# Kernel optimization log

Hardware: AMD Instinct MI355X
Metric: run time of the kernel (lower is better)

## Reference

```python
import jax, jax.numpy as jnp
import numpy as np

WS = 8        # window size (square)
HEADS = 8
DIM = 512
EPS = 1e-5


def _ln(x, g, b):
    m = x.mean(-1, keepdims=True)
    v = x.var(-1, keepdims=True)
    return (x - m) / jnp.sqrt(v + EPS) * g + b


def _bn(x, g, b, m, v):
    # eval-mode BatchNorm2d on NCHW
    sh = (1, -1, 1, 1)
    return (x - m.reshape(sh)) / jnp.sqrt(v.reshape(sh) + EPS) * g.reshape(sh) + b.reshape(sh)


def _win_rev(w, H, W, C):
    # (B*nW, WS*WS, C) -> (B, C, H, W)
    x = w.reshape(-1, H // WS, W // WS, WS, WS, C)
    return x.transpose(0, 5, 1, 3, 2, 4).reshape(-1, C, H, W)


def _win_part(x):
    # (B, C, H, W) -> (B*nW, WS*WS, C)
    B, C, H, W = x.shape
    x = x.reshape(B, C, H // WS, WS, W // WS, WS)
    return x.transpose(0, 2, 4, 3, 5, 1).reshape(-1, WS * WS, C)


def setup_inputs() -> dict:
    key = jax.random.key(0)
    ks = iter(jax.random.split(key, 64))
    def nrm(sh, s=0.02):
        return jax.random.normal(next(ks), sh, jnp.float32) * s
    C, C2, C8 = DIM, DIM // 2, DIM // 8
    B, H, W = 2, 224, 224
    N = WS * WS
    B_ = B * (H // WS) * (W // WS)
    # relative position index (same construction as the torch module)
    coords = np.stack(np.meshgrid(np.arange(WS), np.arange(WS), indexing='ij'))
    cf = coords.reshape(2, -1)
    rel = (cf[:, :, None] - cf[:, None, :]).transpose(1, 2, 0).astype(np.int64)
    rel[:, :, 0] += WS - 1
    rel[:, :, 1] += WS - 1
    rel[:, :, 0] *= 2 * WS - 1
    rel_idx = jnp.asarray(rel.sum(-1), jnp.int32)   # (N, N)
    ones = lambda n: jnp.ones((n,), jnp.float32)
    zeros = lambda n: jnp.zeros((n,), jnp.float32)
    return dict(
        x=jax.random.normal(next(ks), (B_, N, C), jnp.float32),
        w_pa=nrm((C, C2)), b_pa=zeros(C2),
        g_lna=ones(C2) + nrm((C2,), 0.1), b_lna=nrm((C2,), 0.1),
        w_pc=nrm((C, C)), b_pc=zeros(C),
        g_lnc=ones(C) + nrm((C,), 0.1), b_lnc=nrm((C,), 0.1),
        dw_w=nrm((C, 1, 3, 3), 0.1), dw_b=zeros(C),
        g_bn1=ones(C), b_bn1=zeros(C), m_bn1=nrm((C,), 0.1), v_bn1=ones(C),
        ci_w1=nrm((C, C8)), ci_b1=zeros(C8),
        g_bn2=ones(C8), b_bn2=zeros(C8), m_bn2=nrm((C8,), 0.1), v_bn2=ones(C8),
        ci_w2=nrm((C8, C2)), ci_b2=zeros(C2),
        pj_w=nrm((C, C2)), pj_b=zeros(C2),
        g_bn3=ones(C2), b_bn3=zeros(C2), m_bn3=nrm((C2,), 0.1), v_bn3=ones(C2),
        w_qkv=nrm((C2, 3 * C2)), b_qkv=zeros(3 * C2),
        si_w1=nrm((C2, C8)), si_b1=zeros(C8),
        g_bn4=ones(C8), b_bn4=zeros(C8), m_bn4=nrm((C8,), 0.1), v_bn4=ones(C8),
        si_w2=nrm((C8, 1)), si_b2=zeros(1),
        g_lno=ones(C2) + nrm((C2,), 0.1), b_lno=nrm((C2,), 0.1),
        w_out=nrm((C, C)), b_out=zeros(C),
        rpb=nrm(((2 * WS - 1) ** 2, HEADS)),
        rel_idx=rel_idx, H=H, W=W,
    )


def _forward(x, w_pa, b_pa, g_lna, b_lna, w_pc, b_pc, g_lnc, b_lnc,
             dw_w, dw_b, g_bn1, b_bn1, m_bn1, v_bn1,
             ci_w1, ci_b1, g_bn2, b_bn2, m_bn2, v_bn2, ci_w2, ci_b2,
             pj_w, pj_b, g_bn3, b_bn3, m_bn3, v_bn3,
             w_qkv, b_qkv,
             si_w1, si_b1, g_bn4, b_bn4, m_bn4, v_bn4, si_w2, si_b2,
             g_lno, b_lno, w_out, b_out, rpb, rel_idx, H, W):
    B_, N, C = x.shape
    C2 = C // 2
    hd = C2 // HEADS
    scale = hd ** -0.5
    x_att = _ln(x @ w_pa + b_pa, g_lna, b_lna)            # (B_, N, C2)
    x_cnn = _ln(x @ w_pc + b_pc, g_lnc, b_lnc)            # (B_, N, C)
    x_cnn = _win_rev(x_cnn, H, W, C)                      # (B, C, H, W)
    # depthwise 3x3 conv + BN + GELU
    x_cnn = jax.lax.conv_general_dilated(
        x_cnn, dw_w, (1, 1), [(1, 1), (1, 1)],
        feature_group_count=C, dimension_numbers=('NCHW', 'OIHW', 'NCHW')
    ) + dw_b.reshape(1, -1, 1, 1)
    x_cnn = jax.nn.gelu(_bn(x_cnn, g_bn1, b_bn1, m_bn1, v_bn1), approximate=False)
    # channel interaction: global avg pool -> 1x1 conv -> BN -> GELU -> 1x1 conv
    ci = x_cnn.mean((2, 3))                               # (B, C)
    ci = ci @ ci_w1 + ci_b1                               # (B, C/8)
    ci = jax.nn.gelu((ci - m_bn2) / jnp.sqrt(v_bn2 + EPS) * g_bn2 + b_bn2, approximate=False)
    ci = ci @ ci_w2 + ci_b2                               # (B, C2)
    x_cnn = jnp.einsum('bchw,co->bohw', x_cnn, pj_w) + pj_b.reshape(1, -1, 1, 1)  # (B, C2, H, W)
    # windowed multi-head attention
    qkv = (x_att @ w_qkv + b_qkv).reshape(B_, N, 3, HEADS, hd).transpose(2, 0, 3, 1, 4)
    q, k, v = qkv[0], qkv[1], qkv[2]                      # (B_, heads, N, hd)
    B = ci.shape[0]
    gate = jax.nn.sigmoid(ci).reshape(B, 1, HEADS, 1, hd)
    v = (v.reshape(B, -1, HEADS, N, hd) * gate).reshape(B_, HEADS, N, hd)
    attn = jnp.einsum('bhnd,bhmd->bhnm', q * scale, k)    # (B_, heads, N, N)
    bias = rpb[rel_idx[:N, :N].reshape(-1)].reshape(N, N, HEADS).transpose(2, 0, 1)
    attn = jax.nn.softmax(attn + bias[None], axis=-1)
    x_att = jnp.einsum('bhnm,bhmd->bnhd', attn, v).reshape(B_, N, C2)
    # spatial interaction gating of the conv branch
    x_sp = _win_rev(x_att, H, W, C2)                      # (B, C2, H, W)
    si = jnp.einsum('bchw,co->bohw', x_sp, si_w1) + si_b1.reshape(1, -1, 1, 1)
    si = jax.nn.gelu(_bn(si, g_bn4, b_bn4, m_bn4, v_bn4), approximate=False)
    si = jnp.einsum('bchw,co->bohw', si, si_w2) + si_b2.reshape(1, -1, 1, 1)      # (B, 1, H, W)
    x_cnn = _bn(jax.nn.sigmoid(si) * x_cnn, g_bn3, b_bn3, m_bn3, v_bn3)
    x_cnn = _win_part(x_cnn)                              # (B_, N, C2)
    x_att = _ln(x_att, g_lno, b_lno)
    return jnp.concatenate([x_att, x_cnn], axis=-1) @ w_out + b_out


def reference(x, w_pa, b_pa, g_lna, b_lna, w_pc, b_pc, g_lnc, b_lnc,
              dw_w, dw_b, g_bn1, b_bn1, m_bn1, v_bn1,
              ci_w1, ci_b1, g_bn2, b_bn2, m_bn2, v_bn2, ci_w2, ci_b2,
              pj_w, pj_b, g_bn3, b_bn3, m_bn3, v_bn3,
              w_qkv, b_qkv,
              si_w1, si_b1, g_bn4, b_bn4, m_bn4, v_bn4, si_w2, si_b2,
              g_lno, b_lno, w_out, b_out, rpb, rel_idx, H, W):
    return _forward(x, w_pa, b_pa, g_lna, b_lna, w_pc, b_pc, g_lnc, b_lnc,
                    dw_w, dw_b, g_bn1, b_bn1, m_bn1, v_bn1,
                    ci_w1, ci_b1, g_bn2, b_bn2, m_bn2, v_bn2, ci_w2, ci_b2,
                    pj_w, pj_b, g_bn3, b_bn3, m_bn3, v_bn3,
                    w_qkv, b_qkv,
                    si_w1, si_b1, g_bn4, b_bn4, m_bn4, v_bn4, si_w2, si_b2,
                    g_lno, b_lno, w_out, b_out, rpb, rel_idx, H, W)
```

## Files before the change

### kernel.cpp

```cpp
#include <hip/hip_runtime.h>
#include <math.h>

#define EPS 1e-5f
#define MROWS 100352
#define NWIN  1568

typedef __attribute__((ext_vector_type(8))) short bf16x8;
typedef __attribute__((ext_vector_type(4))) float f32x4;

__device__ __forceinline__ unsigned short f2bf(float f) {
  unsigned u = __float_as_uint(f);
  u += 0x7fffu + ((u >> 16) & 1u);
  return (unsigned short)(u >> 16);
}
__device__ __forceinline__ float bf2f(unsigned short s) {
  return __uint_as_float(((unsigned)s) << 16);
}
__device__ __forceinline__ float gelu_exact(float x) {
  return 0.5f * x * (1.f + erff(x * 0.70710678118654752f));
}

#define GLOAD16(gp, lp)                                              \
  __builtin_amdgcn_global_load_lds(                                  \
      (const __attribute__((address_space(1))) void*)(gp),           \
      (__attribute__((address_space(3))) void*)(lp), 16, 0, 0)

template <bool OUTBF>
__global__ __launch_bounds__(256) void gemm_bf16(
    const unsigned short* __restrict__ A, const unsigned short* __restrict__ Bt,
    const float* __restrict__ bias, void* __restrict__ Cout,
    int M, int N, int K) {
  __shared__ unsigned short As[128 * 32];
  __shared__ unsigned short Bs[128 * 32];
  const int tid = threadIdx.x;
  const int lane = tid & 63, wave = tid >> 6;
  const int wr = wave >> 1, wc = wave & 1;
  const int row0 = blockIdx.y * 128, col0 = blockIdx.x * 128;
  const int lrow = tid >> 2, loff = (tid & 3) * 8;
  f32x4 acc[4][4];
#pragma unroll
  for (int m = 0; m < 4; ++m)
#pragma unroll
    for (int n = 0; n < 4; ++n) acc[m][n] = (f32x4){0.f, 0.f, 0.f, 0.f};
  for (int k0 = 0; k0 < K; k0 += 32) {
    __syncthreads();
#pragma unroll
    for (int p = 0; p < 2; ++p) {
      int r = p * 64 + lrow;
      GLOAD16(&A[(size_t)(row0 + r) * K + k0 + loff], &As[r * 32 + loff]);
      GLOAD16(&Bt[(size_t)(col0 + r) * K + k0 + loff], &Bs[r * 32 + loff]);
    }
    __syncthreads();
    const int g8 = (lane >> 4) * 8, rl = lane & 15;
    bf16x8 af[4], bfr[4];
#pragma unroll
    for (int m = 0; m < 4; ++m)
      af[m] = *(const bf16x8*)&As[(wr * 64 + m * 16 + rl) * 32 + g8];
#pragma unroll
    for (int n = 0; n < 4; ++n)
      bfr[n] = *(const bf16x8*)&Bs[(wc * 64 + n * 16 + rl) * 32 + g8];
#pragma unroll
    for (int m = 0; m < 4; ++m)
#pragma unroll
      for (int n = 0; n < 4; ++n)
        acc[m][n] = __builtin_amdgcn_mfma_f32_16x16x32_bf16(af[m], bfr[n],
                                                            acc[m][n], 0, 0, 0);
  }
  const int crow = (lane >> 4) * 4, ccol = lane & 15;
#pragma unroll
  for (int n = 0; n < 4; ++n) {
    const int gc = col0 + wc * 64 + n * 16 + ccol;
    const float bz = bias[gc];
#pragma unroll
    for (int m = 0; m < 4; ++m) {
      const int gr0 = row0 + wr * 64 + m * 16 + crow;
#pragma unroll
      for (int r = 0; r < 4; ++r) {
        float val = acc[m][n][r] + bz;
        if constexpr (OUTBF)
          ((unsigned short*)Cout)[(size_t)(gr0 + r) * N + gc] = f2bf(val);
        else
          ((float*)Cout)[(size_t)(gr0 + r) * N + gc] = val;
      }
    }
  }
}

__global__ __launch_bounds__(256) void gemm_f32a(
    const float* __restrict__ A, const unsigned short* __restrict__ Bt,
    const float* __restrict__ bias, unsigned short* __restrict__ Cout,
    int M, int N, int K) {
  __shared__ unsigned short As[128 * 32];
  __shared__ unsigned short Bs[128 * 32];
  const int tid = threadIdx.x;
  const int lane = tid & 63, wave = tid >> 6;
  const int wr = wave >> 1, wc = wave & 1;
  const int row0 = blockIdx.y * 128, col0 = blockIdx.x * 128;
  const int lrow = tid >> 2, loff = (tid & 3) * 8;
  const int ar = tid >> 1, ac = (tid & 1) * 16;
  f32x4 acc[4][4];
#pragma unroll
  for (int m = 0; m < 4; ++m)
#pragma unroll
    for (int n = 0; n < 4; ++n) acc[m][n] = (f32x4){0.f, 0.f, 0.f, 0.f};
  for (int k0 = 0; k0 < K; k0 += 32) {
    float4 f[4];
#pragma unroll
    for (int i = 0; i < 4; ++i)
      f[i] = *(const float4*)&A[(size_t)(row0 + ar) * K + k0 + ac + i * 4];
    __syncthreads();
#pragma unroll
    for (int p = 0; p < 2; ++p) {
      int r = p * 64 + lrow;
      GLOAD16(&Bt[(size_t)(col0 + r) * K + k0 + loff], &Bs[r * 32 + loff]);
    }
#pragma unroll
    for (int i = 0; i < 4; ++i) {
      ushort4 u = make_ushort4(f2bf(f[i].x), f2bf(f[i].y), f2bf(f[i].z), f2bf(f[i].w));
      *(ushort4*)&As[ar * 32 + ac + i * 4] = u;
    }
    __syncthreads();
    const int g8 = (lane >> 4) * 8, rl = lane & 15;
    bf16x8 af[4], bfr[4];
#pragma unroll
    for (int m = 0; m < 4; ++m)
      af[m] = *(const bf16x8*)&As[(wr * 64 + m * 16 + rl) * 32 + g8];
#pragma unroll
    for (int n = 0; n < 4; ++n)
      bfr[n] = *(const bf16x8*)&Bs[(wc * 64 + n * 16 + rl) * 32 + g8];
#pragma unroll
    for (int m = 0; m < 4; ++m)
#pragma unroll
      for (int n = 0; n < 4; ++n)
        acc[m][n] = __builtin_amdgcn_mfma_f32_16x16x32_bf16(af[m], bfr[n],
                                                            acc[m][n], 0, 0, 0);
  }
  const int crow = (lane >> 4) * 4, ccol = lane & 15;
#pragma unroll
  for (int n = 0; n < 4; ++n) {
    const int gc = col0 + wc * 64 + n * 16 + ccol;
    const float bz = bias[gc];
#pragma unroll
    for (int m = 0; m < 4; ++m) {
      const int gr0 = row0 + wr * 64 + m * 16 + crow;
#pragma unroll
      for (int r = 0; r < 4; ++r)
        Cout[(size_t)(gr0 + r) * N + gc] = f2bf(acc[m][n][r] + bz);
    }
  }
}

__global__ __launch_bounds__(256) void wt_convert(const float* __restrict__ in,
                                                  unsigned short* __restrict__ out,
                                                  int K, int N) {
  int i = blockIdx.x * 256 + threadIdx.x;
  if (i >= K * N) return;
  int n = i / K, k = i - n * K;
  out[i] = f2bf(in[(size_t)k * N + n]);
}

__global__ __launch_bounds__(256) void pack_bias(const float* __restrict__ b_pa,
                                                 const float* __restrict__ b_pc,
                                                 float* __restrict__ out) {
  int t = blockIdx.x * 256 + threadIdx.x;
  if (t < 256) out[t] = b_pa[t];
  else if (t < 768) out[t] = b_pc[t - 256];
}

template <int W>
__global__ __launch_bounds__(256) void ln_rows_bf(
    const unsigned short* __restrict__ in, int istride,
    unsigned short* __restrict__ out,
    const float* __restrict__ g, const float* __restrict__ b) {
  const int row = blockIdx.x * 4 + (threadIdx.x >> 6);
  const int t = threadIdx.x & 63;
  constexpr int NE = W / 64;
  float v[NE];
  const size_t ibase = (size_t)row * istride + t * NE;
  const size_t obase = (size_t)row * W + t * NE;
#pragma unroll
  for (int c4 = 0; c4 < NE / 4; ++c4) {
    ushort4 u = *(const ushort4*)&in[ibase + c4 * 4];
    v[c4 * 4 + 0] = bf2f(u.x); v[c4 * 4 + 1] = bf2f(u.y);
    v[c4 * 4 + 2] = bf2f(u.z); v[c4 * 4 + 3] = bf2f(u.w);
  }
  float s = 0.f, sq = 0.f;
#pragma unroll
  for (int j = 0; j < NE; ++j) { s += v[j]; sq += v[j] * v[j]; }
#pragma unroll
  for (int off = 32; off >= 1; off >>= 1) {
    s += __shfl_xor(s, off);
    sq += __shfl_xor(sq, off);
  }
  const float mean = s * (1.f / W);
  const float var = sq * (1.f / W) - mean * mean;
  const float rstd = rsqrtf(var + EPS);
#pragma unroll
  for (int c4 = 0; c4 < NE / 4; ++c4) {
    int c = t * NE + c4 * 4;
    ushort4 o = make_ushort4(
        f2bf((v[c4 * 4 + 0] - mean) * rstd * g[c + 0] + b[c + 0]),
        f2bf((v[c4 * 4 + 1] - mean) * rstd * g[c + 1] + b[c + 1]),
        f2bf((v[c4 * 4 + 2] - mean) * rstd * g[c + 2] + b[c + 2]),
        f2bf((v[c4 * 4 + 3] - mean) * rstd * g[c + 3] + b[c + 3]));
    *(ushort4*)&out[obase + c4 * 4] = o;
  }
}

__global__ __launch_bounds__(256) void dwconv_bn_gelu(
    const unsigned short* __restrict__ xin, const float* __restrict__ wgt9,
    const float* __restrict__ dwb, const float* __restrict__ g1,
    const float* __restrict__ b1, const float* __restrict__ m1,
    const float* __restrict__ v1, unsigned short* __restrict__ outp,
    float* __restrict__ ci_part) {
  __shared__ unsigned short tile[100 * 128];
  __shared__ float psum[8 * 128];
  const int b_ = blockIdx.x;
  const int b = b_ / 784, win = b_ % 784;
  const int wi = win / 28, wj = win % 28;
  const int h0 = wi * 8 - 1, w0 = wj * 8 - 1;
  const int tid = threadIdx.x;
  const int c4 = (tid & 31) * 4;
  const int pg = tid >> 5;
  for (int chunk = 0; chunk < 4; ++chunk) {
    const int c0 = chunk * 128;
    __syncthreads();
#pragma unroll
    for (int it = 0; it < 7; ++it) {
      int idx = it * 256 + tid;
      if (idx < 1600) {
        int p = idx >> 4;
        int ch8 = (idx & 15) * 8;
        int ph = h0 + p / 10, pw = w0 + p % 10;
        uint4 val = {0u, 0u, 0u, 0u};
        if (ph >= 0 && ph < 224 && pw >= 0 && pw < 224) {
          int bs = b * 784 + (ph >> 3) * 28 + (pw >> 3);
          int n = ((ph & 7) << 3) | (pw & 7);
          val = *(const uint4*)&xin[(size_t)(bs * 64 + n) * 512 + c0 + ch8];
        }
        *(uint4*)&tile[p * 128 + ch8] = val;
      }
    }
    __syncthreads();
    float wreg[9][4];
    float scale[4], shift[4], bias0[4];
#pragma unroll
    for (int j = 0; j < 4; ++j) {
      int cc = c0 + c4 + j;
#pragma unroll
      for (int k = 0; k < 9; ++k) wreg[k][j] = wgt9[cc * 9 + k];
      scale[j] = g1[cc] * rsqrtf(v1[cc] + EPS);
      shift[j] = b1[cc] - m1[cc] * scale[j];
      bias0[j] = dwb[cc];
    }
    float cs0 = 0.f, cs1 = 0.f, cs2 = 0.f, cs3 = 0.f;
    for (int q = 0; q < 8; ++q) {
      const int qq = pg * 8 + q;
      const int r = qq >> 3, cc_ = qq & 7;
      float a0 = bias0[0], a1 = bias0[1], a2 = bias0[2], a3 = bias0[3];
#pragma unroll
      for (int dr = 0; dr < 3; ++dr)
#pragma unroll
        for (int dc = 0; dc < 3; ++dc) {
          ushort4 u = *(const ushort4*)&tile[((r + dr) * 10 + cc_ + dc) * 128 + c4];
          const int k = dr * 3 + dc;
          a0 += bf2f(u.x) * wreg[k][0];
          a1 += bf2f(u.y) * wreg[k][1];
          a2 += bf2f(u.z) * wreg[k][2];
          a3 += bf2f(u.w) * wreg[k][3];
        }
      float g0 = gelu_exact(a0 * scale[0] + shift[0]);
      float g1v = gelu_exact(a1 * scale[1] + shift[1]);
      float g2v = gelu_exact(a2 * scale[2] + shift[2]);
      float g3v = gelu_exact(a3 * scale[3] + shift[3]);
      cs0 += g0; cs1 += g1v; cs2 += g2v; cs3 += g3v;
      *(ushort4*)&outp[(size_t)(b_ * 64 + qq) * 512 + c0 + c4] =
          make_ushort4(f2bf(g0), f2bf(g1v), f2bf(g2v), f2bf(g3v));
    }
    *(float4*)&psum[pg * 128 + c4] = make_float4(cs0, cs1, cs2, cs3);
    __syncthreads();
    if (tid < 128) {
      float s = 0.f;
#pragma unroll
      for (int g = 0; g < 8; ++g) s += psum[g * 128 + tid];
      ci_part[(size_t)b_ * 512 + c0 + tid] = s;
    }
  }
}

__global__ __launch_bounds__(512) void ci_reduce(const float* __restrict__ ci_part,
                                                 float* __restrict__ ci_mean) {
  const int b = blockIdx.x, c = threadIdx.x;
  float s = 0.f;
  for (int w = 0; w < 784; ++w) s += ci_part[(size_t)(b * 784 + w) * 512 + c];
  ci_mean[b * 512 + c] = s * (1.f / 50176.f);
}

__global__ __launch_bounds__(512) void ci_gate(
    const float* __restrict__ ci_mean, const float* __restrict__ w1,
    const float* __restrict__ bi1, const float* __restrict__ g2,
    const float* __restrict__ b2, const float* __restrict__ m2,
    const float* __restrict__ v2, const float* __restrict__ w2,
    const float* __restrict__ bi2, float* __restrict__ gate) {
  __shared__ float cm[1024];
  __shared__ float c1[128];
  const int t = threadIdx.x;
  cm[t] = ci_mean[t];
  cm[t + 512] = ci_mean[t + 512];
  __syncthreads();
  if (t < 128) {
    int b = t >> 6, j = t & 63;
    float acc = bi1[j];
    for (int c = 0; c < 512; ++c) acc += cm[b * 512 + c] * w1[c * 64 + j];
    float sc = g2[j] * rsqrtf(v2[j] + EPS);
    c1[t] = gelu_exact((acc - m2[j]) * sc + b2[j]);
  }
  __syncthreads();
  {
    int b = t >> 8, o = t & 255;
    float acc = bi2[o];
#pragma unroll
    for (int j = 0; j < 64; ++j) acc += c1[b * 64 + j] * w2[j * 256 + o];
    gate[b * 256 + o] = 1.f / (1.f + expf(-acc));
  }
}

__global__ __launch_bounds__(256) void bias_pre(const float* __restrict__ rpb,
                                                const int* __restrict__ rel,
                                                float* __restrict__ biasf) {
  int i = blockIdx.x * 256 + threadIdx.x;
  if (i >= 4096) return;
  int r = rel[i];
#pragma unroll
  for (int h = 0; h < 8; ++h) biasf[h * 4096 + i] = rpb[r * 8 + h];
}

__global__ __launch_bounds__(256) void attn_mfma(
    const unsigned short* __restrict__ qkv,
    const float* __restrict__ gate,
    const float* __restrict__ biasf,
    unsigned short* __restrict__ outp) {
  __shared__ unsigned short lds[4 * (64 * 68 + 32 * 68)];
  const int w = blockIdx.x;
  const int b = w / 784;
  const int tid = threadIdx.x, lane = tid & 63, wave = tid >> 6;
  unsigned short* p_lds = lds + wave * (64 * 68 + 32 * 68);
  unsigned short* vT = p_lds + 64 * 68;
  const int l15 = lane & 15, l4 = lane >> 4;
  const float scale = 0.17677669529663687f;
  for (int hh = 0; hh < 2; ++hh) {
    const int h = wave * 2 + hh;
    {
      const float* gh = &gate[b * 256 + h * 32];
      const size_t vbase = ((size_t)w * 64 + lane) * 768 + 512 + h * 32;
#pragma unroll
      for (int c = 0; c < 4; ++c) {
        uint4 vv = *(const uint4*)&qkv[vbase + c * 8];
        float4 gA = *(const float4*)&gh[c * 8];
        float4 gB = *(const float4*)&gh[c * 8 + 4];
        unsigned vw[4] = {vv.x, vv.y, vv.z, vv.w};
        float gg[8] = {gA.x, gA.y, gA.z, gA.w, gB.x, gB.y, gB.z, gB.w};
#pragma unroll
        for (int j = 0; j < 4; ++j) {
          int d = c * 8 + j * 2;
          vT[(d + 0) * 68 + lane] = f2bf(__uint_as_float(vw[j] << 16) * gg[j * 2]);
          vT[(d + 1) * 68 + lane] =
              f2bf(__uint_as_float(vw[j] & 0xffff0000u) * gg[j * 2 + 1]);
        }
      }
    }
    bf16x8 kf[4], qf[4];
    const size_t qkbase = (size_t)w * 64 * 768 + h * 32 + l4 * 8;
#pragma unroll
    for (int t = 0; t < 4; ++t) {
      kf[t] = *(const bf16x8*)&qkv[qkbase + (size_t)(t * 16 + l15) * 768 + 256];
      qf[t] = *(const bf16x8*)&qkv[qkbase + (size_t)(t * 16 + l15) * 768];
    }
    f32x4 s[4][4];
#pragma unroll
    for (int mt = 0; mt < 4; ++mt)
#pragma unroll
      for (int nt = 0; nt < 4; ++nt) s[mt][nt] = (f32x4){0.f, 0.f, 0.f, 0.f};
#pragma unroll
    for (int mt = 0; mt < 4; ++mt)
#pragma unroll
      for (int nt = 0; nt < 4; ++nt)
        s[mt][nt] = __builtin_amdgcn_mfma_f32_16x16x32_bf16(kf[mt], qf[nt],
                                                            s[mt][nt], 0, 0, 0);
    float inv_s[4];
#pragma unroll
    for (int nt = 0; nt < 4; ++nt) {
      float mx = -1e30f;
#pragma unroll
      for (int mt = 0; mt < 4; ++mt) {
        float4 b4 = *(const float4*)&biasf[(h * 64 + nt * 16 + l15) * 64 +
                                           mt * 16 + l4 * 4];
        s[mt][nt][0] = s[mt][nt][0] * scale + b4.x;
        s[mt][nt][1] = s[mt][nt][1] * scale + b4.y;
        s[mt][nt][2] = s[mt][nt][2] * scale + b4.z;
        s[mt][nt][3] = s[mt][nt][3] * scale + b4.w;
#pragma unroll
        for (int r = 0; r < 4; ++r) mx = fmaxf(mx, s[mt][nt][r]);
      }
      mx = fmaxf(mx, __shfl_xor(mx, 16));
      mx = fmaxf(mx, __shfl_xor(mx, 32));
      float sum = 0.f;
#pragma unroll
      for (int mt = 0; mt < 4; ++mt)
#pragma unroll
        for (int r = 0; r < 4; ++r) {
          float e = __expf(s[mt][nt][r] - mx);
          s[mt][nt][r] = e;
          sum += e;
        }
      sum += __shfl_xor(sum, 16);
      sum += __shfl_xor(sum, 32);
      inv_s[nt] = 1.f / sum;
    }
#pragma unroll
    for (int nt = 0; nt < 4; ++nt)
#pragma unroll
      for (int mt = 0; mt < 4; ++mt) {
        ushort4 pk = make_ushort4(f2bf(s[mt][nt][0] * inv_s[nt]),
                                  f2bf(s[mt][nt][1] * inv_s[nt]),
                                  f2bf(s[mt][nt][2] * inv_s[nt]),
                                  f2bf(s[mt][nt][3] * inv_s[nt]));
        *(ushort4*)&p_lds[(nt * 16 + l15) * 68 + mt * 16 + l4 * 4] = pk;
      }
    f32x4 o[4][2];
#pragma unroll
    for (int i = 0; i < 4; ++i)
#pragma unroll
      for (int dt = 0; dt < 2; ++dt) o[i][dt] = (f32x4){0.f, 0.f, 0.f, 0.f};
#pragma unroll
    for (int ks = 0; ks < 2; ++ks) {
      bf16x8 pa[4], vf[2];
#pragma unroll
      for (int i = 0; i < 4; ++i) {
        const unsigned short* pp = &p_lds[(i * 16 + l15) * 68 + ks * 32 + l4 * 8];
        union { bf16x8 v; ushort4 u[2]; } tmp;
        tmp.u[0] = *(const ushort4*)pp;
        tmp.u[1] = *(const ushort4*)(pp + 4);
        pa[i] = tmp.v;
      }
#pragma unroll
      for (int dt = 0; dt < 2; ++dt) {
        const unsigned short* vp = &vT[(dt * 16 + l15) * 68 + ks * 32 + l4 * 8];
        union { bf16x8 v; ushort4 u[2]; } tmp;
        tmp.u[0] = *(const ushort4*)vp;
        tmp.u[1] = *(const ushort4*)(vp + 4);
        vf[dt] = tmp.v;
      }
#pragma unroll
      for (int i = 0; i < 4; ++i)
#pragma unroll
        for (int dt = 0; dt < 2; ++dt)
          o[i][dt] = __builtin_amdgcn_mfma_f32_16x16x32_bf16(pa[i], vf[dt],
                                                             o[i][dt], 0, 0, 0);
    }
#pragma unroll
    for (int i = 0; i < 4; ++i)
#pragma unroll
      for (int dt = 0; dt < 2; ++dt)
#pragma unroll
        for (int r = 0; r < 4; ++r)
          outp[((size_t)w * 64 + i * 16 + l4 * 4 + r) * 256 + h * 32 +
               dt * 16 + l15] = f2bf(o[i][dt][r]);
  }
}

__global__ __launch_bounds__(256) void si_ln_concat(
    const unsigned short* __restrict__ xatt, const unsigned short* __restrict__ xpj,
    const float* __restrict__ w1, const float* __restrict__ bi1,
    const float* __restrict__ g4, const float* __restrict__ b4v,
    const float* __restrict__ m4, const float* __restrict__ v4,
    const float* __restrict__ w2, const float* __restrict__ bi2,
    const float* __restrict__ g3, const float* __restrict__ b3v,
    const float* __restrict__ m3, const float* __restrict__ v3,
    const float* __restrict__ glno, const float* __restrict__ blno,
    unsigned short* __restrict__ outc) {
  __shared__ float xr[16 * 256];
  __shared__ float s1s[16 * 64];
  __shared__ float sig[16];
  const int t = threadIdx.x;
  const int row0 = blockIdx.x * 16;
#pragma unroll
  for (int i = 0; i < 2; ++i) {
    int idx = i * 256 + t;
    int pr = idx >> 5, pc = (idx & 31) * 8;
    const unsigned short* src = &xatt[(size_t)(row0 + pr) * 256 + pc];
    ushort4 a = *(const ushort4*)src;
    ushort4 c = *(const ushort4*)(src + 4);
    float* dst = &xr[pr * 256 + pc];
    dst[0] = bf2f(a.x); dst[1] = bf2f(a.y); dst[2] = bf2f(a.z); dst[3] = bf2f(a.w);
    dst[4] = bf2f(c.x); dst[5] = bf2f(c.y); dst[6] = bf2f(c.z); dst[7] = bf2f(c.w);
  }
  __syncthreads();
  {
    const int j = t & 63, pg = t >> 6;
    float acc[4];
    const float bj = bi1[j];
#pragma unroll
    for (int i = 0; i < 4; ++i) acc[i] = bj;
    for (int cc = 0; cc < 256; ++cc) {
      float wv = w1[cc * 64 + j];
#pragma unroll
      for (int i = 0; i < 4; ++i) acc[i] += xr[(pg * 4 + i) * 256 + cc] * wv;
    }
    const float sc4 = g4[j] * rsqrtf(v4[j] + EPS);
    const float m4j = m4[j], b4j = b4v[j];
#pragma unroll
    for (int i = 0; i < 4; ++i)
      s1s[(pg * 4 + i) * 64 + j] = gelu_exact((acc[i] - m4j) * sc4 + b4j);
  }
  __syncthreads();
  if (t < 16) {
    float a2 = bi2[0];
#pragma unroll
    for (int jj = 0; jj < 64; ++jj) a2 += s1s[t * 64 + jj] * w2[jj];
    sig[t] = 1.f / (1.f + expf(-a2));
  }
  __syncthreads();
  {
    const int p = t >> 4, l = t & 15;
    float4 v4s[4];
    float s = 0.f, sq = 0.f;
#pragma unroll
    for (int cq = 0; cq < 4; ++cq) {
      float4 x4 = *(const float4*)&xr[p * 256 + cq * 64 + l * 4];
      v4s[cq] = x4;
      s += x4.x + x4.y + x4.z + x4.w;
      sq += x4.x * x4.x + x4.y * x4.y + x4.z * x4.z + x4.w * x4.w;
    }
#pragma unroll
    for (int off = 8; off >= 1; off >>= 1) {
      s += __shfl_xor(s, off);
      sq += __shfl_xor(sq, off);
    }
    const float mean = s * (1.f / 256.f);
    const float var = sq * (1.f / 256.f) - mean * mean;
    const float rstd = rsqrtf(var + EPS);
    const size_t orow = (size_t)(row0 + p) * 512;
#pragma unroll
    for (int cq = 0; cq < 4; ++cq) {
      int c = cq * 64 + l * 4;
      float4 x4 = v4s[cq];
      *(ushort4*)&outc[orow + c] = make_ushort4(
          f2bf((x4.x - mean) * rstd * glno[c + 0] + blno[c + 0]),
          f2bf((x4.y - mean) * rstd * glno[c + 1] + blno[c + 1]),
          f2bf((x4.z - mean) * rstd * glno[c + 2] + blno[c + 2]),
          f2bf((x4.w - mean) * rstd * glno[c + 3] + blno[c + 3]));
    }
    const float sg = sig[p];
#pragma unroll
    for (int cq = 0; cq < 4; ++cq) {
      int c = cq * 64 + l * 4;
      ushort4 pu = *(const ushort4*)&xpj[(size_t)(row0 + p) * 256 + c];
      float px = bf2f(pu.x), py = bf2f(pu.y), pz = bf2f(pu.z), pw = bf2f(pu.w);
      float sc0 = g3[c + 0] * rsqrtf(v3[c + 0] + EPS);
      float sc1 = g3[c + 1] * rsqrtf(v3[c + 1] + EPS);
      float sc2 = g3[c + 2] * rsqrtf(v3[c + 2] + EPS);
      float sc3 = g3[c + 3] * rsqrtf(v3[c + 3] + EPS);
      *(ushort4*)&outc[orow + 256 + c] = make_ushort4(
          f2bf(sg * px * sc0 + (b3v[c + 0] - m3[c + 0] * sc0)),
          f2bf(sg * py * sc1 + (b3v[c + 1] - m3[c + 1] * sc1)),
          f2bf(sg * pz * sc2 + (b3v[c + 2] - m3[c + 2] * sc2)),
          f2bf(sg * pw * sc3 + (b3v[c + 3] - m3[c + 3] * sc3)));
    }
  }
}

extern "C" void kernel_launch(void* const* d_in, const int* in_sizes, int n_in,
                              void* d_out, int out_size, void* d_ws, size_t ws_size,
                              hipStream_t stream) {
  const float* x     = (const float*)d_in[0];
  const float* w_pa  = (const float*)d_in[1];
  const float* b_pa  = (const float*)d_in[2];
  const float* g_lna = (const float*)d_in[3];
  const float* b_lna = (const float*)d_in[4];
  const float* w_pc  = (const float*)d_in[5];
  const float* b_pc  = (const float*)d_in[6];
  const float* g_lnc = (const float*)d_in[7];
  const float* b_lnc = (const float*)d_in[8];
  const float* dw_w  = (const float*)d_in[9];
  const float* dw_b  = (const float*)d_in[10];
  const float* g_bn1 = (const float*)d_in[11];
  const float* b_bn1 = (const float*)d_in[12];
  const float* m_bn1 = (const float*)d_in[13];
  const float* v_bn1 = (const float*)d_in[14];
  const float* ci_w1 = (const float*)d_in[15];
  const float* ci_b1 = (const float*)d_in[16];
  const float* g_bn2 = (const float*)d_in[17];
  const float* b_bn2 = (const float*)d_in[18];
  const float* m_bn2 = (const float*)d_in[19];
  const float* v_bn2 = (const float*)d_in[20];
  const float* ci_w2 = (const float*)d_in[21];
  const float* ci_b2 = (const float*)d_in[22];
  const float* pj_w  = (const float*)d_in[23];
  const float* pj_b  = (const float*)d_in[24];
  const float* g_bn3 = (const float*)d_in[25];
  const float* b_bn3 = (const float*)d_in[26];
  const float* m_bn3 = (const float*)d_in[27];
  const float* v_bn3 = (const float*)d_in[28];
  const float* w_qkv = (const float*)d_in[29];
  const float* b_qkv = (const float*)d_in[30];
  const float* si_w1 = (const float*)d_in[31];
  const float* si_b1 = (const float*)d_in[32];
  const float* g_bn4 = (const float*)d_in[33];
  const float* b_bn4 = (const float*)d_in[34];
  const float* m_bn4 = (const float*)d_in[35];
  const float* v_bn4 = (const float*)d_in[36];
  const float* si_w2 = (const float*)d_in[37];
  const float* si_b2 = (const float*)d_in[38];
  const float* g_lno = (const float*)d_in[39];
  const float* b_lno = (const float*)d_in[40];
  const float* w_out = (const float*)d_in[41];
  const float* b_out = (const float*)d_in[42];
  const float* rpb   = (const float*)d_in[43];
  const int*   rel   = (const int*)d_in[44];

  char* ws = (char*)d_ws;
  unsigned short* G12BF = (unsigned short*)(ws + 0);
  unsigned short* QKVBF = (unsigned short*)(ws + 0);
  unsigned short* A1BF  = (unsigned short*)(ws + 154140672ull);
  unsigned short* ATTBF = (unsigned short*)(ws + 154140672ull);
  unsigned short* C1BF  = (unsigned short*)(ws + 205520896ull);
  unsigned short* CAT   = (unsigned short*)(ws + 205520896ull);
  unsigned short* CVBF  = (unsigned short*)(ws + 308281344ull);
  unsigned short* PJBF  = (unsigned short*)(ws + 411041792ull);
  float*          CIP   = (float*)(ws + 462422016ull);
  float*          CIM   = (float*)(ws + 465633280ull);
  float*          GATE  = (float*)(ws + 465637376ull);
  float*          B12   = (float*)(ws + 465639424ull);
  float*          BIASF = (float*)(ws + 465642496ull);
  unsigned short* WT    = (unsigned short*)(ws + 465773568ull);
  unsigned short* WpaT  = WT + 0;
  unsigned short* WpcT  = WT + 131072;
  unsigned short* PjT   = WT + 393216;
  unsigned short* QkvT  = WT + 524288;
  unsigned short* OutT  = WT + 720896;

  const int M = MROWS;
  dim3 b256(256), b512(512);

  wt_convert<<<512, b256, 0, stream>>>(w_pa, WpaT, 512, 256);
  wt_convert<<<1024, b256, 0, stream>>>(w_pc, WpcT, 512, 512);
  wt_convert<<<512, b256, 0, stream>>>(pj_w, PjT, 512, 256);
  wt_convert<<<768, b256, 0, stream>>>(w_qkv, QkvT, 256, 768);
  wt_convert<<<1024, b256, 0, stream>>>(w_out, OutT, 512, 512);
  pack_bias<<<3, b256, 0, stream>>>(b_pa, b_pc, B12);

  gemm_f32a<<<dim3(6, M / 128), b256, 0, stream>>>(x, WpaT, B12, G12BF, M, 768, 512);
  ln_rows_bf<256><<<M / 4, b256, 0, stream>>>(G12BF, 768, A1BF, g_lna, b_lna);
  ln_rows_bf<512><<<M / 4, b256, 0, stream>>>(G12BF + 256, 768, C1BF, g_lnc, b_lnc);

  dwconv_bn_gelu<<<NWIN, b256, 0, stream>>>(C1BF, dw_w, dw_b, g_bn1, b_bn1, m_bn1,
                                            v_bn1, CVBF, CIP);
  ci_reduce<<<2, b512, 0, stream>>>(CIP, CIM);
  ci_gate<<<1, b512, 0, stream>>>(CIM, ci_w1, ci_b1, g_bn2, b_bn2, m_bn2, v_bn2,
                                  ci_w2, ci_b2, GATE);
  bias_pre<<<16, b256, 0, stream>>>(rpb, rel, BIASF);

  gemm_bf16<true><<<dim3(2, M / 128), b256, 0, stream>>>(CVBF, PjT, pj_b, PJBF, M, 256, 512);

  gemm_bf16<true><<<dim3(6, M / 128), b256, 0, stream>>>(A1BF, QkvT, b_qkv, QKVBF, M, 768, 256);

  attn_mfma<<<NWIN, b256, 0, stream>>>(QKVBF, GATE, BIASF, ATTBF);

  si_ln_concat<<<M / 16, b256, 0, stream>>>(ATTBF, PJBF, si_w1, si_b1, g_bn4, b_bn4,
                                            m_bn4, v_bn4, si_w2, si_b2, g_bn3,
                                            b_bn3, m_bn3, v_bn3, g_lno, b_lno, CAT);

  gemm_bf16<false><<<dim3(4, M / 128), b256, 0, stream>>>(CAT, OutT, b_out,
                                                          (float*)d_out, M, 512, 512);
}
```

Baseline: 860.6 us.

## Replace GEMMs with 256x256 double-buffered swizzled-LDS kernel and pre-convert input

All four projection GEMMs now use a new 512-thread kernel with 256x256 tiles and K-step 64. It double-buffers LDS with async global-to-LDS loads interleaved with MFMA phases, uses an XOR-swizzled LDS layout to avoid bank conflicts, and remaps workgroups for cache locality. The fp32-input GEMM is replaced by a separate fp32-to-bf16 conversion pass followed by the bf16 kernel. This adds an extra memory pass over x and uses 128KB of LDS per block, which limits occupancy.

```diff
diff --git a/kernel.cpp b/kernel.cpp
--- a/kernel.cpp
+++ b/kernel.cpp
@@ -25,55 +25,114 @@
       (const __attribute__((address_space(1))) void*)(gp),           \
       (__attribute__((address_space(3))) void*)(lp), 16, 0, 0)
 
+__device__ __forceinline__ void stage_half256(
+    const unsigned short* __restrict__ base, int r0, int K, int kk,
+    unsigned short* lds, int ldsbase, int tid) {
+#pragma unroll
+  for (int inst = 0; inst < 2; ++inst) {
+    int r = inst * 64 + (tid >> 3);
+    int cb = ((tid & 7) << 4) ^ ((r & 7) << 4);
+    const unsigned short* src = base + (size_t)(r0 + r) * K + kk + (cb >> 1);
+    GLOAD16(src, &lds[ldsbase + inst * 4096 + tid * 8]);
+  }
+}
+
+__device__ __forceinline__ bf16x8 frag_read256(const unsigned short* lds,
+                                               int tilebase, int r_t, int cbyte) {
+  int off = r_t * 128 + cbyte;
+  int phys = off ^ ((r_t & 7) << 4);
+  return *(const bf16x8*)&lds[tilebase + (phys >> 1)];
+}
+
 template <bool OUTBF>
-__global__ __launch_bounds__(256) void gemm_bf16(
+__global__ __launch_bounds__(512) void gemm256(
     const unsigned short* __restrict__ A, const unsigned short* __restrict__ Bt,
     const float* __restrict__ bias, void* __restrict__ Cout,
     int M, int N, int K) {
-  __shared__ unsigned short As[128 * 32];
-  __shared__ unsigned short Bs[128 * 32];
+  __shared__ unsigned short lds[65536];
   const int tid = threadIdx.x;
   const int lane = tid & 63, wave = tid >> 6;
-  const int wr = wave >> 1, wc = wave & 1;
-  const int row0 = blockIdx.y * 128, col0 = blockIdx.x * 128;
-  const int lrow = tid >> 2, loff = (tid & 3) * 8;
-  f32x4 acc[4][4];
-#pragma unroll
-  for (int m = 0; m < 4; ++m)
+  const int wr = wave >> 2;
+  const int wcn = wave & 3;
+  int bx, by;
+  {
+    const int nwg = gridDim.x * gridDim.y;
+    int n = blockIdx.y * gridDim.x + blockIdx.x;
+    int w = ((nwg & 7) == 0) ? ((n & 7) * (nwg >> 3) + (n >> 3)) : n;
+    by = w / gridDim.x;
+    bx = w - by * gridDim.x;
+  }
+  const int row0 = by * 256, col0 = bx * 256;
+  const int rl = lane & 15, qd = lane >> 4;
+  f32x4 acc[8][4];
+#pragma unroll
+  for (int m = 0; m < 8; ++m)
 #pragma unroll
     for (int n = 0; n < 4; ++n) acc[m][n] = (f32x4){0.f, 0.f, 0.f, 0.f};
-  for (int k0 = 0; k0 < K; k0 += 32) {
-    __syncthreads();
-#pragma unroll
-    for (int p = 0; p < 2; ++p) {
-      int r = p * 64 + lrow;
-      GLOAD16(&A[(size_t)(row0 + r) * K + k0 + loff], &As[r * 32 + loff]);
-      GLOAD16(&Bt[(size_t)(col0 + r) * K + k0 + loff], &Bs[r * 32 + loff]);
-    }
-    __syncthreads();
-    const int g8 = (lane >> 4) * 8, rl = lane & 15;
-    bf16x8 af[4], bfr[4];
-#pragma unroll
-    for (int m = 0; m < 4; ++m)
-      af[m] = *(const bf16x8*)&As[(wr * 64 + m * 16 + rl) * 32 + g8];
-#pragma unroll
-    for (int n = 0; n < 4; ++n)
-      bfr[n] = *(const bf16x8*)&Bs[(wc * 64 + n * 16 + rl) * 32 + g8];
-#pragma unroll
-    for (int m = 0; m < 4; ++m)
-#pragma unroll
-      for (int n = 0; n < 4; ++n)
-        acc[m][n] = __builtin_amdgcn_mfma_f32_16x16x32_bf16(af[m], bfr[n],
-                                                            acc[m][n], 0, 0, 0);
-  }
-  const int crow = (lane >> 4) * 4, ccol = lane & 15;
+
+  const int KT = K >> 6;
+  stage_half256(A, row0, K, 0, lds, 0, tid);
+  stage_half256(A, row0 + 128, K, 0, lds, 8192, tid);
+  stage_half256(Bt, col0, K, 0, lds, 16384, tid);
+  stage_half256(Bt, col0 + 128, K, 0, lds, 24576, tid);
+
+  for (int kt = 0; kt < KT; ++kt) {
+    const int b = kt & 1;
+    const int abase = b * 32768, bbase = b * 32768 + 16384;
+    const int nb = b ^ 1;
+    const int kkn = (kt + 1) << 6;
+    const bool last = (kt == KT - 1);
+    bf16x8 bfr[4][2];
+#pragma unroll
+    for (int p = 0; p < 4; ++p) {
+      if (!last) {
+        if (p == 0)      stage_half256(A, row0, K, kkn, lds, nb * 32768, tid);
+        else if (p == 1) stage_half256(A, row0 + 128, K, kkn, lds, nb * 32768 + 8192, tid);
+        else if (p == 2) stage_half256(Bt, col0, K, kkn, lds, nb * 32768 + 16384, tid);
+        else             stage_half256(Bt, col0 + 128, K, kkn, lds, nb * 32768 + 24576, tid);
+      }
+      if (p == 0) {
+        if (!last) asm volatile("s_waitcnt vmcnt(2)" ::: "memory");
+        else       asm volatile("s_waitcnt vmcnt(0)" ::: "memory");
+      }
+      __builtin_amdgcn_s_barrier();
+      __builtin_amdgcn_sched_barrier(0);
+      if (p == 0) {
+#pragma unroll
+        for (int n = 0; n < 4; ++n)
+#pragma unroll
+          for (int ks = 0; ks < 2; ++ks)
+            bfr[n][ks] = frag_read256(lds, bbase, wcn * 64 + n * 16 + rl,
+                                      ks * 64 + qd * 16);
+      }
+      bf16x8 af[2][2];
+#pragma unroll
+      for (int i = 0; i < 2; ++i)
+#pragma unroll
+        for (int ks = 0; ks < 2; ++ks)
+          af[i][ks] = frag_read256(lds, abase, wr * 128 + (2 * p + i) * 16 + rl,
+                                   ks * 64 + qd * 16);
+      __builtin_amdgcn_s_setprio(1);
+#pragma unroll
+      for (int i = 0; i < 2; ++i)
+#pragma unroll
+        for (int n = 0; n < 4; ++n)
+#pragma unroll
+          for (int ks = 0; ks < 2; ++ks)
+            acc[2 * p + i][n] = __builtin_amdgcn_mfma_f32_16x16x32_bf16(
+                af[i][ks], bfr[n][ks], acc[2 * p + i][n], 0, 0, 0);
+      __builtin_amdgcn_s_setprio(0);
+      __builtin_amdgcn_s_barrier();
+    }
+  }
+  const int crow = qd * 4, ccol = rl;
 #pragma unroll
   for (int n = 0; n < 4; ++n) {
-    const int gc = col0 + wc * 64 + n * 16 + ccol;
+    const int gc = col0 + wcn * 64 + n * 16 + ccol;
     const float bz = bias[gc];
 #pragma unroll
-    for (int m = 0; m < 4; ++m) {
-      const int gr0 = row0 + wr * 64 + m * 16 + crow;
+    for (int m = 0; m < 8; ++m) {
+      const int gr0 = row0 + wr * 128 + m * 16 + crow;
 #pragma unroll
       for (int r = 0; r < 4; ++r) {
         float val = acc[m][n][r] + bz;
@@ -82,70 +141,6 @@
         else
           ((float*)Cout)[(size_t)(gr0 + r) * N + gc] = val;
       }
-    }
-  }
-}
-
-__global__ __launch_bounds__(256) void gemm_f32a(
-    const float* __restrict__ A, const unsigned short* __restrict__ Bt,
-    const float* __restrict__ bias, unsigned short* __restrict__ Cout,
-    int M, int N, int K) {
-  __shared__ unsigned short As[128 * 32];
-  __shared__ unsigned short Bs[128 * 32];
-  const int tid = threadIdx.x;
-  const int lane = tid & 63, wave = tid >> 6;
-  const int wr = wave >> 1, wc = wave & 1;
-  const int row0 = blockIdx.y * 128, col0 = blockIdx.x * 128;
-  const int lrow = tid >> 2, loff = (tid & 3) * 8;
-  const int ar = tid >> 1, ac = (tid & 1) * 16;
-  f32x4 acc[4][4];
-#pragma unroll
-  for (int m = 0; m < 4; ++m)
-#pragma unroll
-    for (int n = 0; n < 4; ++n) acc[m][n] = (f32x4){0.f, 0.f, 0.f, 0.f};
-  for (int k0 = 0; k0 < K; k0 += 32) {
-    float4 f[4];
-#pragma unroll
-    for (int i = 0; i < 4; ++i)
-      f[i] = *(const float4*)&A[(size_t)(row0 + ar) * K + k0 + ac + i * 4];
-    __syncthreads();
-#pragma unroll
-    for (int p = 0; p < 2; ++p) {
-      int r = p * 64 + lrow;
-      GLOAD16(&Bt[(size_t)(col0 + r) * K + k0 + loff], &Bs[r * 32 + loff]);
-    }
-#pragma unroll
-    for (int i = 0; i < 4; ++i) {
-      ushort4 u = make_ushort4(f2bf(f[i].x), f2bf(f[i].y), f2bf(f[i].z), f2bf(f[i].w));
-      *(ushort4*)&As[ar * 32 + ac + i * 4] = u;
-    }
-    __syncthreads();
-    const int g8 = (lane >> 4) * 8, rl = lane & 15;
-    bf16x8 af[4], bfr[4];
-#pragma unroll
-    for (int m = 0; m < 4; ++m)
-      af[m] = *(const bf16x8*)&As[(wr * 64 + m * 16 + rl) * 32 + g8];
-#pragma unroll
-    for (int n = 0; n < 4; ++n)
-      bfr[n] = *(const bf16x8*)&Bs[(wc * 64 + n * 16 + rl) * 32 + g8];
-#pragma unroll
-    for (int m = 0; m < 4; ++m)
-#pragma unroll
-      for (int n = 0; n < 4; ++n)
-        acc[m][n] = __builtin_amdgcn_mfma_f32_16x16x32_bf16(af[m], bfr[n],
-                                                            acc[m][n], 0, 0, 0);
-  }
-  const int crow = (lane >> 4) * 4, ccol = lane & 15;
-#pragma unroll
-  for (int n = 0; n < 4; ++n) {
-    const int gc = col0 + wc * 64 + n * 16 + ccol;
-    const float bz = bias[gc];
-#pragma unroll
-    for (int m = 0; m < 4; ++m) {
-      const int gr0 = row0 + wr * 64 + m * 16 + crow;
-#pragma unroll
-      for (int r = 0; r < 4; ++r)
-        Cout[(size_t)(gr0 + r) * N + gc] = f2bf(acc[m][n][r] + bz);
     }
   }
 }
@@ -165,6 +160,17 @@
   int t = blockIdx.x * 256 + threadIdx.x;
   if (t < 256) out[t] = b_pa[t];
   else if (t < 768) out[t] = b_pc[t - 256];
+}
+
+__global__ __launch_bounds__(256) void cvt_bf16(const float* __restrict__ in,
+                                                unsigned short* __restrict__ out,
+                                                int n8) {
+  int i = blockIdx.x * 256 + threadIdx.x;
+  if (i >= n8) return;
+  float4 a = ((const float4*)in)[i * 2];
+  float4 b = ((const float4*)in)[i * 2 + 1];
+  ((ushort4*)out)[i * 2] = make_ushort4(f2bf(a.x), f2bf(a.y), f2bf(a.z), f2bf(a.w));
+  ((ushort4*)out)[i * 2 + 1] = make_ushort4(f2bf(b.x), f2bf(b.y), f2bf(b.z), f2bf(b.w));
 }
 
 template <int W>
@@ -626,6 +632,7 @@
   unsigned short* ATTBF = (unsigned short*)(ws + 154140672ull);
   unsigned short* C1BF  = (unsigned short*)(ws + 205520896ull);
   unsigned short* CAT   = (unsigned short*)(ws + 205520896ull);
+  unsigned short* XBF   = (unsigned short*)(ws + 308281344ull);
   unsigned short* CVBF  = (unsigned short*)(ws + 308281344ull);
   unsigned short* PJBF  = (unsigned short*)(ws + 411041792ull);
   float*          CIP   = (float*)(ws + 462422016ull);
@@ -650,7 +657,10 @@
   wt_convert<<<1024, b256, 0, stream>>>(w_out, OutT, 512, 512);
   pack_bias<<<3, b256, 0, stream>>>(b_pa, b_pc, B12);
 
-  gemm_f32a<<<dim3(6, M / 128), b256, 0, stream>>>(x, WpaT, B12, G12BF, M, 768, 512);
+  cvt_bf16<<<(M * 512 / 8 + 255) / 256, b256, 0, stream>>>(x, XBF, M * 512 / 8);
+
+  gemm256<true><<<dim3(3, M / 256), dim3(512), 0, stream>>>(XBF, WpaT, B12, G12BF,
+                                                            M, 768, 512);
   ln_rows_bf<256><<<M / 4, b256, 0, stream>>>(G12BF, 768, A1BF, g_lna, b_lna);
   ln_rows_bf<512><<<M / 4, b256, 0, stream>>>(G12BF + 256, 768, C1BF, g_lnc, b_lnc);
 
@@ -661,9 +671,11 @@
                                   ci_w2, ci_b2, GATE);
   bias_pre<<<16, b256, 0, stream>>>(rpb, rel, BIASF);
 
-  gemm_bf16<true><<<dim3(2, M / 128), b256, 0, stream>>>(CVBF, PjT, pj_b, PJBF, M, 256, 512);
-
-  gemm_bf16<true><<<dim3(6, M / 128), b256, 0, stream>>>(A1BF, QkvT, b_qkv, QKVBF, M, 768, 256);
+  gemm256<true><<<dim3(1, M / 256), dim3(512), 0, stream>>>(CVBF, PjT, pj_b, PJBF,
+                                                            M, 256, 512);
+
+  gemm256<true><<<dim3(3, M / 256), dim3(512), 0, stream>>>(A1BF, QkvT, b_qkv, QKVBF,
+                                                            M, 768, 256);
 
   attn_mfma<<<NWIN, b256, 0, stream>>>(QKVBF, GATE, BIASF, ATTBF);
 
@@ -671,6 +683,6 @@
                                             m_bn4, v_bn4, si_w2, si_b2, g_bn3,
                                             b_bn3, m_bn3, v_bn3, g_lno, b_lno, CAT);
 
-  gemm_bf16<false><<<dim3(4, M / 128), b256, 0, stream>>>(CAT, OutT, b_out,
-                                                          (float*)d_out, M, 512, 512);
-}
+  gemm256<false><<<dim3(2, M / 256), dim3(512), 0, stream>>>(CAT, OutT, b_out,
+                                                             (float*)d_out, M, 512, 512);
+}
```

New measurement: 843.2 us. -2.0%, faster.
